# Optimization experiments

Hardware: AMD Instinct MI355X
Metric: run time of the kernel (lower is better)

## Reference

```python
import jax, jax.numpy as jnp
import numpy as np

B, T, D = 2, 1024, 4096
N, K, H = 32, 8, 128  # query heads, kv heads, head_dim
SLOTS = 4096
ROPE_THETA = 500000.0


def apply_rope(x, positions, head_dim, theta):
    # x: [B, heads, T, H], positions: [B, T]
    half = head_dim // 2
    inv_freq = 1.0 / (theta ** (jnp.arange(0, half, dtype=jnp.float32) / half * 2.0 * 0.5 * 2))
    inv_freq = 1.0 / (theta ** (jnp.arange(0, head_dim, 2, dtype=jnp.float32) / head_dim))  # [half]
    ang = positions.astype(jnp.float32)[:, :, None] * inv_freq[None, None, :]  # [B, T, half]
    cos = jnp.cos(ang)[:, None, :, :]  # [B, 1, T, half]
    sin = jnp.sin(ang)[:, None, :, :]
    x1, x2 = x[..., :half], x[..., half:]
    return jnp.concatenate([x1 * cos - x2 * sin, x2 * cos + x1 * sin], axis=-1)


def update_cache(cache, write_indices, kv):
    # cache: [K, SLOTS, H]; kv: [B, K, T, H]; write_indices: [B*T] flat slot ids
    flat = kv.transpose(1, 0, 2, 3).reshape(kv.shape[1], -1, kv.shape[3])  # [K, B*T, H]
    return cache.at[:, write_indices, :].set(flat)


def setup_inputs() -> dict:
    key = jax.random.key(0)
    ks = jax.random.split(key, 6)
    scale = 0.02
    x = jax.random.normal(ks[0], (B, T, D), jnp.float32)
    wq = jax.random.normal(ks[1], (N, D, H), jnp.float32) * scale
    wk = jax.random.normal(ks[2], (K, D, H), jnp.float32) * scale
    wv = jax.random.normal(ks[3], (K, D, H), jnp.float32) * scale
    wo = jax.random.normal(ks[4], (N, H, D), jnp.float32) * scale
    positions = jnp.tile(jnp.arange(T, dtype=jnp.int32)[None, :], (B, 1))
    k_cache = jnp.zeros((K, SLOTS, H), jnp.float32)
    v_cache = jnp.zeros((K, SLOTS, H), jnp.float32)
    write_indices = jnp.arange(B * T, dtype=jnp.int32)
    return {"x": x, "positions": positions, "wq": wq, "wk": wk, "wv": wv,
            "wo": wo, "k_cache": k_cache, "v_cache": v_cache,
            "write_indices": write_indices}


def reference(x, positions, wq, wk, wv, wo, k_cache, v_cache, write_indices):
    # QKV projections
    q = jnp.einsum('btd,ndh->bnth', x, wq)          # [B, N, T, H]
    k = jnp.einsum('btd,kdh->bkth', x, wk)          # [B, K, T, H]
    v = jnp.einsum('btd,kdh->bkth', x, wv)
    # RoPE, then scale q (matches module: rope before scaling)
    q = apply_rope(q, positions, H, ROPE_THETA) * (H ** -0.5)
    k = apply_rope(k, positions, H, ROPE_THETA)
    # KV-cache scatter update (prefill path)
    k_cache_new = update_cache(k_cache, write_indices, k)
    v_cache_new = update_cache(v_cache, write_indices, v)
    # GQA repeat + causal flash attention
    rep = N // K
    kr = jnp.repeat(k, rep, axis=1)                 # [B, N, T, H]
    vr = jnp.repeat(v, rep, axis=1)
    scores = jnp.einsum('bnth,bnsh->bnts', q, kr)   # [B, N, T, T]
    causal = jnp.tril(jnp.ones((T, T), bool))
    scores = jnp.where(causal[None, None], scores, jnp.finfo(scores.dtype).min)
    probs = jax.nn.softmax(scores, axis=-1)
    attn = jnp.einsum('bnts,bnsh->bnth', probs, vr) # [B, N, T, H]
    o = jnp.einsum('bnth,nhd->btd', attn, wo)       # [B, T, D]
    return (k_cache_new, v_cache_new, o)
```

## Files before the change

### kernel.cpp

```cpp
#include <hip/hip_runtime.h>

typedef unsigned short u16;
typedef float fx4 __attribute__((ext_vector_type(4)));
typedef __bf16 bfx8 __attribute__((ext_vector_type(8)));

#define NSLOTS 4096
#define NEG_INF (-1e30f)
#define QSCALE 0.12751879523486166f

__device__ __forceinline__ u16 f2bf(float f) {
    union { float f; unsigned u; } v; v.f = f;
    unsigned u = v.u;
    unsigned r = (u + 0x7FFFu + ((u >> 16) & 1u)) >> 16;
    return (u16)r;
}
__device__ __forceinline__ float bf2f(u16 h) {
    union { unsigned u; float f; } v; v.u = ((unsigned)h) << 16; return v.f;
}
__device__ __forceinline__ void gll16(const void* g, void* l) {
    __builtin_amdgcn_global_load_lds((__attribute__((address_space(1))) void*)(g),
                                     (__attribute__((address_space(3))) void*)(l),
                                     16, 0, 0);
}

__device__ __forceinline__ void transpose_body(u16 (*t)[72],
                                               const float* __restrict__ ih,
                                               u16* __restrict__ oh, int R, int C,
                                               int r0, int c0) {
    int tid = threadIdx.x;
    int rr = tid >> 4, c4 = tid & 15;
#pragma unroll
    for (int i = 0; i < 4; ++i) {
        int r = rr + i * 16;
        float4 v = *(const float4*)(ih + (size_t)(r0 + r) * C + c0 + c4 * 4);
        t[c4 * 4 + 0][r] = f2bf(v.x);
        t[c4 * 4 + 1][r] = f2bf(v.y);
        t[c4 * 4 + 2][r] = f2bf(v.z);
        t[c4 * 4 + 3][r] = f2bf(v.w);
    }
    __syncthreads();
    int rr2 = tid >> 3, c8 = tid & 7;
#pragma unroll
    for (int i = 0; i < 2; ++i) {
        int r = rr2 + i * 32;
        *(uint4*)(oh + (size_t)(c0 + r) * R + r0 + c8 * 8) = *(uint4*)&t[r][c8 * 8];
    }
}

__global__ __launch_bounds__(256) void prep(
    const float* __restrict__ x, const float* __restrict__ wq,
    const float* __restrict__ wk, const float* __restrict__ wv,
    const float* __restrict__ wo, const float* __restrict__ kc,
    const float* __restrict__ vc, u16* __restrict__ x_bf,
    u16* __restrict__ wqkvT, u16* __restrict__ woT, float* __restrict__ cache_out) {
    __shared__ __align__(16) u16 t[64][72];
    int id = blockIdx.x;
    int tid = threadIdx.x;
    if (id < 4096) {
        int f4i = id * 512 + tid * 2;
        const float4* src = (id < 2048) ? (const float4*)kc + f4i
                                        : (const float4*)vc + (f4i - 1048576);
        float4 a = src[0], b = src[1];
        float4* dst = (float4*)cache_out + f4i;
        dst[0] = a;
        dst[1] = b;
    } else if (id < 8192) {
        int i = ((id - 4096) * 256 + tid) * 8;
        float4 a = *(const float4*)(x + i);
        float4 b = *(const float4*)(x + i + 4);
        u16 tmp[8] = {f2bf(a.x), f2bf(a.y), f2bf(a.z), f2bf(a.w),
                      f2bf(b.x), f2bf(b.y), f2bf(b.z), f2bf(b.w)};
        *(uint4*)(x_bf + i) = *(uint4*)tmp;
    } else if (id < 14336) {
        int id3 = id - 8192;
        int z = id3 >> 7;
        int rem = id3 & 127;
        int by = rem >> 1, bx = rem & 1;
        const float* in = (z < 32) ? wq + (size_t)z * 524288
                                   : (z < 40) ? wk + (size_t)(z - 32) * 524288
                                              : wv + (size_t)(z - 40) * 524288;
        transpose_body(t, in, wqkvT + (size_t)z * 524288, 4096, 128, by * 64,
                       bx * 64);
    } else {
        int id4 = id - 14336;
        int bx = id4 & 63, by = id4 >> 6;
        transpose_body(t, wo, woT, 4096, 4096, by * 64, bx * 64);
    }
}

template <int OUTF32>
__global__ __launch_bounds__(256) void gemm_bt(const u16* __restrict__ A,
                                               const u16* __restrict__ Bt,
                                               void* __restrict__ Cv,
                                               int M, int N, int Kd) {
    __shared__ __align__(16) u16 As[128 * 64];
    __shared__ __align__(16) u16 Bs[128 * 64];
    const int tid = threadIdx.x;
    const int lane = tid & 63;
    const int wave = tid >> 6;
    const int wm = (wave >> 1) * 64;
    const int wn = (wave & 1) * 64;
    const int m0 = blockIdx.y * 128;
    const int n0 = blockIdx.x * 128;
    const int quad = lane >> 4;
    const int l15 = lane & 15;
    const int srow = lane >> 3;
    const int sc8 = (lane & 7) ^ srow;

    fx4 zero = {0.f, 0.f, 0.f, 0.f};
    fx4 acc[4][4];
#pragma unroll
    for (int i = 0; i < 4; ++i)
#pragma unroll
        for (int j = 0; j < 4; ++j) acc[i][j] = zero;

    for (int k0 = 0; k0 < Kd; k0 += 64) {
        __syncthreads();
#pragma unroll
        for (int i = 0; i < 4; ++i) {
            int c = wave * 4 + i;
            gll16(A + (size_t)(m0 + c * 8 + srow) * Kd + (k0 + sc8 * 8), &As[c * 512]);
            gll16(Bt + (size_t)(n0 + c * 8 + srow) * Kd + (k0 + sc8 * 8), &Bs[c * 512]);
        }
        __syncthreads();
#pragma unroll
        for (int ks = 0; ks < 2; ++ks) {
            bfx8 af[4], bf[4];
#pragma unroll
            for (int t = 0; t < 4; ++t) {
                int row = wm + t * 16 + l15;
                int r7 = row & 7;
                int k8 = (ks * 4 + quad) ^ r7;
                af[t] = *(const bfx8*)&As[(row >> 3) * 512 + r7 * 64 + k8 * 8];
                int rowb = wn + t * 16 + l15;
                int r7b = rowb & 7;
                int k8b = (ks * 4 + quad) ^ r7b;
                bf[t] = *(const bfx8*)&Bs[(rowb >> 3) * 512 + r7b * 64 + k8b * 8];
            }
#pragma unroll
            for (int tm = 0; tm < 4; ++tm)
#pragma unroll
                for (int tn = 0; tn < 4; ++tn)
                    acc[tm][tn] = __builtin_amdgcn_mfma_f32_16x16x32_bf16(
                        af[tm], bf[tn], acc[tm][tn], 0, 0, 0);
        }
    }
#pragma unroll
    for (int tm = 0; tm < 4; ++tm)
#pragma unroll
        for (int tn = 0; tn < 4; ++tn) {
            int col = n0 + wn + tn * 16 + l15;
#pragma unroll
            for (int r = 0; r < 4; ++r) {
                int row = m0 + wm + tm * 16 + quad * 4 + r;
                if (OUTF32)
                    ((float*)Cv)[(size_t)row * N + col] = acc[tm][tn][r];
                else
                    ((u16*)Cv)[(size_t)row * N + col] = f2bf(acc[tm][tn][r]);
            }
        }
}

__global__ __launch_bounds__(256) void rope_tv(
    const u16* __restrict__ qkv, const int* __restrict__ positions,
    const int* __restrict__ wi, u16* __restrict__ qb, u16* __restrict__ kb,
    float* __restrict__ kcache, float* __restrict__ vcache, u16* __restrict__ vt) {
    __shared__ __align__(16) u16 Ts[64 * 64];
    int id = blockIdx.x;
    int tid = threadIdx.x;
    if (id < 24576) {
        int m = id / 12;
        int j2 = (id % 12) * 256 + tid;
        int head = j2 >> 6;
        int hp = (j2 & 63) * 2;
        int b = m >> 10, t = m & 1023;
        const u16* row = qkv + (size_t)m * 6144 + head * 128;
        unsigned sv = *(const unsigned*)(row + hp);
        float v0 = bf2f((u16)sv), v1 = bf2f((u16)(sv >> 16));
        if (head < 40) {
            int i = hp & 63;
            float p = (float)positions[m];
            float ang0 = p * __expf(-0.20503693f * (float)i);
            float ang1 = ang0 * 0.81461709f;
            float c0, s0, c1, s1;
            __sincosf(ang0, &s0, &c0);
            __sincosf(ang1, &s1, &c1);
            unsigned ov = *(const unsigned*)(row + (hp ^ 64));
            float w0 = bf2f((u16)ov), w1 = bf2f((u16)(ov >> 16));
            float o0, o1;
            if (hp < 64) { o0 = v0 * c0 - w0 * s0; o1 = v1 * c1 - w1 * s1; }
            else         { o0 = v0 * c0 + w0 * s0; o1 = v1 * c1 + w1 * s1; }
            if (head < 32) {
                o0 *= QSCALE; o1 *= QSCALE;
                u16 t2[2] = {f2bf(o0), f2bf(o1)};
                *(unsigned*)(qb + ((size_t)(b * 32 + head) * 1024 + t) * 128 + hp) =
                    *(unsigned*)t2;
            } else {
                int kh = head - 32;
                u16 t2[2] = {f2bf(o0), f2bf(o1)};
                *(unsigned*)(kb + ((size_t)(b * 8 + kh) * 1024 + t) * 128 + hp) =
                    *(unsigned*)t2;
                float2 f2 = {o0, o1};
                *(float2*)(kcache + ((size_t)kh * NSLOTS + wi[m]) * 128 + hp) = f2;
            }
        } else {
            int kh = head - 40;
            float2 f2 = {v0, v1};
            *(float2*)(vcache + ((size_t)kh * NSLOTS + wi[m]) * 128 + hp) = f2;
        }
    } else {
        int idx = id - 24576;
        int tt = idx & 15;
        int hh = (idx >> 4) & 1;
        int bkh = idx >> 5;
        int bq = bkh >> 3, kh = bkh & 7;
        const u16* src =
            qkv + (size_t)(bq * 1024 + tt * 64) * 6144 + 5120 + kh * 128 + hh * 64;
        {
            int r = tid >> 3, c8 = tid & 7;
#pragma unroll
            for (int i = 0; i < 2; ++i) {
                int rr = r + i * 32;
                *(uint4*)&Ts[rr * 64 + ((c8 ^ (rr & 7)) * 8)] =
                    *(const uint4*)(src + (size_t)rr * 6144 + c8 * 8);
            }
        }
        __syncthreads();
        int h = tid & 63, t8 = tid >> 6;
        int h8 = h >> 3, h7 = h & 7;
        u16* dst =
            vt + (size_t)bkh * 131072 + (size_t)(hh * 64 + h) * 1024 + tt * 64;
#pragma unroll
        for (int i = 0; i < 2; ++i) {
            int tb = t8 + i * 4;
            u16 tmp[8];
#pragma unroll
            for (int j = 0; j < 8; ++j)
                tmp[j] = Ts[(tb * 8 + j) * 64 + ((h8 ^ j) * 8 + h7)];
            *(uint4*)(dst + tb * 8) = *(uint4*)tmp;
        }
    }
}

__global__ __launch_bounds__(256) void flash_attn(const u16* __restrict__ qb,
                                                  const u16* __restrict__ kb,
                                                  const u16* __restrict__ vt,
                                                  u16* __restrict__ attn) {
    const int qt = blockIdx.x;
    const int n = blockIdx.y;
    const int b = blockIdx.z;
    const int kh = n >> 2;
    const int tid = threadIdx.x;
    const int lane = tid & 63;
    const int wave = tid >> 6;
    const int quad = lane >> 4;
    const int l15 = lane & 15;

    __shared__ __align__(16) u16 Ks[64 * 128];
    __shared__ __align__(16) u16 Vs[128 * 64];
    __shared__ __align__(16) u16 Ps[4][16 * 72];

    const u16* qbase =
        qb + ((size_t)(b * 32 + n) * 1024 + qt * 64 + wave * 16 + l15) * 128;
    bfx8 qf[4];
#pragma unroll
    for (int ks = 0; ks < 4; ++ks)
        qf[ks] = *(const bfx8*)(qbase + ks * 32 + quad * 8);

    const u16* kbase = kb + (size_t)(b * 8 + kh) * 131072;
    const u16* vbase = vt + (size_t)(b * 8 + kh) * 131072;

    const int kl = wave * 4 + (lane >> 4);
    const int kh8 = (lane & 15) ^ (kl & 7);
    const int hl = wave * 8 + (lane >> 3);
    const int vk8 = (lane & 7) ^ (hl & 7);

    fx4 zero = {0.f, 0.f, 0.f, 0.f};
    fx4 o[8];
#pragma unroll
    for (int i = 0; i < 8; ++i) o[i] = zero;
    float mrow[4], lrow[4];
#pragma unroll
    for (int r = 0; r < 4; ++r) { mrow[r] = NEG_INF; lrow[r] = 0.f; }

    for (int kt = 0; kt <= qt; ++kt) {
        __syncthreads();
        const u16* ksrc = kbase + (size_t)kt * 64 * 128;
        const u16* vsrc = vbase + kt * 64;
#pragma unroll
        for (int i = 0; i < 4; ++i)
            gll16(ksrc + (size_t)(i * 16 + kl) * 128 + kh8 * 8,
                  &Ks[(i * 16 + wave * 4) * 128]);
#pragma unroll
        for (int i = 0; i < 4; ++i)
            gll16(vsrc + (size_t)(i * 32 + hl) * 1024 + vk8 * 8,
                  &Vs[(i * 32 + wave * 8) * 64]);
        __syncthreads();

        fx4 sAcc[4];
#pragma unroll
        for (int t = 0; t < 4; ++t) sAcc[t] = zero;
#pragma unroll
        for (int ks = 0; ks < 4; ++ks)
#pragma unroll
            for (int tn = 0; tn < 4; ++tn) {
                int key = tn * 16 + l15;
                bfx8 kf =
                    *(const bfx8*)&Ks[key * 128 + (((ks * 4 + quad) ^ (key & 7)) * 8)];
                sAcc[tn] = __builtin_amdgcn_mfma_f32_16x16x32_bf16(qf[ks], kf,
                                                                   sAcc[tn], 0, 0, 0);
            }
        if (kt == qt) {
#pragma unroll
            for (int tn = 0; tn < 4; ++tn)
#pragma unroll
                for (int r = 0; r < 4; ++r) {
                    int qrow = wave * 16 + quad * 4 + r;
                    int krow = tn * 16 + l15;
                    if (krow > qrow) sAcc[tn][r] = NEG_INF;
                }
        }
        float alpha[4];
#pragma unroll
        for (int r = 0; r < 4; ++r) {
            float mx = fmaxf(fmaxf(sAcc[0][r], sAcc[1][r]),
                             fmaxf(sAcc[2][r], sAcc[3][r]));
#pragma unroll
            for (int d = 1; d < 16; d <<= 1) mx = fmaxf(mx, __shfl_xor(mx, d));
            float mnew = fmaxf(mrow[r], mx);
            alpha[r] = exp2f(mrow[r] - mnew);
            mrow[r] = mnew;
            float rs = 0.f;
#pragma unroll
            for (int tn = 0; tn < 4; ++tn) {
                float p = exp2f(sAcc[tn][r] - mnew);
                sAcc[tn][r] = p;
                rs += p;
            }
#pragma unroll
            for (int d = 1; d < 16; d <<= 1) rs += __shfl_xor(rs, d);
            lrow[r] = lrow[r] * alpha[r] + rs;
        }
#pragma unroll
        for (int tn = 0; tn < 4; ++tn)
#pragma unroll
            for (int r = 0; r < 4; ++r)
                Ps[wave][(quad * 4 + r) * 72 + tn * 16 + l15] = f2bf(sAcc[tn][r]);
#pragma unroll
        for (int ht = 0; ht < 8; ++ht)
#pragma unroll
            for (int r = 0; r < 4; ++r) o[ht][r] *= alpha[r];
#pragma unroll
        for (int ks2 = 0; ks2 < 2; ++ks2) {
            bfx8 pf = *(const bfx8*)&Ps[wave][l15 * 72 + ks2 * 32 + quad * 8];
#pragma unroll
            for (int ht = 0; ht < 8; ++ht) {
                int h = ht * 16 + l15;
                bfx8 vf =
                    *(const bfx8*)&Vs[h * 64 + (((ks2 * 4 + quad) ^ (h & 7)) * 8)];
                o[ht] = __builtin_amdgcn_mfma_f32_16x16x32_bf16(pf, vf, o[ht], 0, 0, 0);
            }
        }
    }
    float inv_l[4];
#pragma unroll
    for (int r = 0; r < 4; ++r) inv_l[r] = 1.f / lrow[r];
#pragma unroll
    for (int ht = 0; ht < 8; ++ht)
#pragma unroll
        for (int r = 0; r < 4; ++r) {
            int t = qt * 64 + wave * 16 + quad * 4 + r;
            int col = n * 128 + ht * 16 + l15;
            attn[((size_t)(b * 1024 + t)) * 4096 + col] = f2bf(o[ht][r] * inv_l[r]);
        }
}

extern "C" void kernel_launch(void* const* d_in, const int* in_sizes, int n_in,
                              void* d_out, int out_size, void* d_ws, size_t ws_size,
                              hipStream_t stream) {
    const float* x = (const float*)d_in[0];
    const int* pos = (const int*)d_in[1];
    const float* wq = (const float*)d_in[2];
    const float* wk = (const float*)d_in[3];
    const float* wv = (const float*)d_in[4];
    const float* wo = (const float*)d_in[5];
    const float* kc = (const float*)d_in[6];
    const float* vc = (const float*)d_in[7];
    const int* wi = (const int*)d_in[8];

    float* kc_out = (float*)d_out;
    float* vc_out = kc_out + 4194304;
    float* o_out = vc_out + 4194304;

    u16* wsp = (u16*)d_ws;
    u16* x_bf  = wsp;
    u16* wqkvT = x_bf + 8388608;
    u16* woT   = wqkvT + 25165824;
    u16* qkv   = woT + 16777216;
    u16* qbuf  = qkv + 12582912;
    u16* kbuf  = qbuf + 8388608;
    u16* vtb   = kbuf + 2097152;
    u16* attn  = vtb + 2097152;

    prep<<<18432, 256, 0, stream>>>(x, wq, wk, wv, wo, kc, vc, x_bf, wqkvT, woT,
                                    kc_out);
    gemm_bt<0><<<dim3(48, 16), 256, 0, stream>>>(x_bf, wqkvT, qkv, 2048, 6144, 4096);
    rope_tv<<<25088, 256, 0, stream>>>(qkv, pos, wi, qbuf, kbuf, kc_out, vc_out, vtb);
    flash_attn<<<dim3(16, 32, 2), 256, 0, stream>>>(qbuf, kbuf, vtb, attn);
    gemm_bt<1><<<dim3(32, 16), 256, 0, stream>>>(attn, woT, o_out, 2048, 4096, 4096);
}
```

Before: 543.7 us.

## Pair causal query tiles per block, swizzle transpose LDS, defer row-sum reduction

Flash attention now launches half as many blocks. Each block handles query tile p and then tile 15-p, so every block does the same amount of causal work instead of some blocks doing far more than others. The per-iteration row-sum shuffle reduction is deferred to a single reduction at the end. The weight transpose in prep uses an XOR-swizzled LDS layout to avoid bank conflicts, and the cache copy switches to coalesced strided float4 accesses. The grid shrinks to 512 blocks, which may reduce occupancy on a GPU with many CUs.

```diff
diff --git a/kernel.cpp b/kernel.cpp
--- a/kernel.cpp
+++ b/kernel.cpp
@@ -23,7 +23,7 @@
                                      16, 0, 0);
 }
 
-__device__ __forceinline__ void transpose_body(u16 (*t)[72],
+__device__ __forceinline__ void transpose_body(u16* __restrict__ t,
                                                const float* __restrict__ ih,
                                                u16* __restrict__ oh, int R, int C,
                                                int r0, int c0) {
@@ -31,19 +31,22 @@
     int rr = tid >> 4, c4 = tid & 15;
 #pragma unroll
     for (int i = 0; i < 4; ++i) {
-        int r = rr + i * 16;
-        float4 v = *(const float4*)(ih + (size_t)(r0 + r) * C + c0 + c4 * 4);
-        t[c4 * 4 + 0][r] = f2bf(v.x);
-        t[c4 * 4 + 1][r] = f2bf(v.y);
-        t[c4 * 4 + 2][r] = f2bf(v.z);
-        t[c4 * 4 + 3][r] = f2bf(v.w);
+        int b = rr + i * 16;
+        float4 v = *(const float4*)(ih + (size_t)(r0 + b) * C + c0 + c4 * 4);
+        u16 vals[4] = {f2bf(v.x), f2bf(v.y), f2bf(v.z), f2bf(v.w)};
+#pragma unroll
+        for (int j = 0; j < 4; ++j) {
+            int a = c4 * 4 + j;
+            t[a * 72 + (((b >> 3) ^ (a & 7)) << 3) + (b & 7)] = vals[j];
+        }
     }
     __syncthreads();
     int rr2 = tid >> 3, c8 = tid & 7;
 #pragma unroll
     for (int i = 0; i < 2; ++i) {
-        int r = rr2 + i * 32;
-        *(uint4*)(oh + (size_t)(c0 + r) * R + r0 + c8 * 8) = *(uint4*)&t[r][c8 * 8];
+        int a = rr2 + i * 32;
+        *(uint4*)(oh + (size_t)(c0 + a) * R + r0 + c8 * 8) =
+            *(uint4*)&t[a * 72 + ((c8 ^ (a & 7)) << 3)];
     }
 }
 
@@ -53,17 +56,17 @@
     const float* __restrict__ wo, const float* __restrict__ kc,
     const float* __restrict__ vc, u16* __restrict__ x_bf,
     u16* __restrict__ wqkvT, u16* __restrict__ woT, float* __restrict__ cache_out) {
-    __shared__ __align__(16) u16 t[64][72];
+    __shared__ __align__(16) u16 t[64 * 72];
     int id = blockIdx.x;
     int tid = threadIdx.x;
     if (id < 4096) {
-        int f4i = id * 512 + tid * 2;
+        int f4i = id * 512 + tid;
         const float4* src = (id < 2048) ? (const float4*)kc + f4i
                                         : (const float4*)vc + (f4i - 1048576);
-        float4 a = src[0], b = src[1];
+        float4 a = src[0], b = src[256];
         float4* dst = (float4*)cache_out + f4i;
         dst[0] = a;
-        dst[1] = b;
+        dst[256] = b;
     } else if (id < 8192) {
         int i = ((id - 4096) * 256 + tid) * 8;
         float4 a = *(const float4*)(x + i);
@@ -89,10 +92,10 @@
 }
 
 template <int OUTF32>
-__global__ __launch_bounds__(256) void gemm_bt(const u16* __restrict__ A,
-                                               const u16* __restrict__ Bt,
-                                               void* __restrict__ Cv,
-                                               int M, int N, int Kd) {
+__device__ __forceinline__ void gemm_core(const u16* __restrict__ A,
+                                          const u16* __restrict__ Bt,
+                                          void* __restrict__ Cv,
+                                          int M, int N, int Kd) {
     __shared__ __align__(16) u16 As[128 * 64];
     __shared__ __align__(16) u16 Bs[128 * 64];
     const int tid = threadIdx.x;
@@ -159,6 +162,19 @@
                     ((u16*)Cv)[(size_t)row * N + col] = f2bf(acc[tm][tn][r]);
             }
         }
+}
+
+__global__ __launch_bounds__(256) void gemm_qkv(const u16* __restrict__ A,
+                                                const u16* __restrict__ Bt,
+                                                u16* __restrict__ C, int M, int N,
+                                                int Kd) {
+    gemm_core<0>(A, Bt, C, M, N, Kd);
+}
+__global__ __launch_bounds__(256) void gemm_out(const u16* __restrict__ A,
+                                                const u16* __restrict__ Bt,
+                                                float* __restrict__ C, int M, int N,
+                                                int Kd) {
+    gemm_core<1>(A, Bt, C, M, N, Kd);
 }
 
 __global__ __launch_bounds__(256) void rope_tv(
@@ -246,7 +262,7 @@
                                                   const u16* __restrict__ kb,
                                                   const u16* __restrict__ vt,
                                                   u16* __restrict__ attn) {
-    const int qt = blockIdx.x;
+    const int p = blockIdx.x;
     const int n = blockIdx.y;
     const int b = blockIdx.z;
     const int kh = n >> 2;
@@ -260,13 +276,6 @@
     __shared__ __align__(16) u16 Vs[128 * 64];
     __shared__ __align__(16) u16 Ps[4][16 * 72];
 
-    const u16* qbase =
-        qb + ((size_t)(b * 32 + n) * 1024 + qt * 64 + wave * 16 + l15) * 128;
-    bfx8 qf[4];
-#pragma unroll
-    for (int ks = 0; ks < 4; ++ks)
-        qf[ks] = *(const bfx8*)(qbase + ks * 32 + quad * 8);
-
     const u16* kbase = kb + (size_t)(b * 8 + kh) * 131072;
     const u16* vbase = vt + (size_t)(b * 8 + kh) * 131072;
 
@@ -276,103 +285,118 @@
     const int vk8 = (lane & 7) ^ (hl & 7);
 
     fx4 zero = {0.f, 0.f, 0.f, 0.f};
-    fx4 o[8];
-#pragma unroll
-    for (int i = 0; i < 8; ++i) o[i] = zero;
-    float mrow[4], lrow[4];
-#pragma unroll
-    for (int r = 0; r < 4; ++r) { mrow[r] = NEG_INF; lrow[r] = 0.f; }
-
-    for (int kt = 0; kt <= qt; ++kt) {
-        __syncthreads();
-        const u16* ksrc = kbase + (size_t)kt * 64 * 128;
-        const u16* vsrc = vbase + kt * 64;
-#pragma unroll
-        for (int i = 0; i < 4; ++i)
-            gll16(ksrc + (size_t)(i * 16 + kl) * 128 + kh8 * 8,
-                  &Ks[(i * 16 + wave * 4) * 128]);
-#pragma unroll
-        for (int i = 0; i < 4; ++i)
-            gll16(vsrc + (size_t)(i * 32 + hl) * 1024 + vk8 * 8,
-                  &Vs[(i * 32 + wave * 8) * 64]);
-        __syncthreads();
-
-        fx4 sAcc[4];
-#pragma unroll
-        for (int t = 0; t < 4; ++t) sAcc[t] = zero;
+
+    for (int ph = 0; ph < 2; ++ph) {
+        const int qt = ph ? (15 - p) : p;
+        const u16* qbase =
+            qb + ((size_t)(b * 32 + n) * 1024 + qt * 64 + wave * 16 + l15) * 128;
+        bfx8 qf[4];
 #pragma unroll
         for (int ks = 0; ks < 4; ++ks)
-#pragma unroll
-            for (int tn = 0; tn < 4; ++tn) {
-                int key = tn * 16 + l15;
-                bfx8 kf =
-                    *(const bfx8*)&Ks[key * 128 + (((ks * 4 + quad) ^ (key & 7)) * 8)];
-                sAcc[tn] = __builtin_amdgcn_mfma_f32_16x16x32_bf16(qf[ks], kf,
-                                                                   sAcc[tn], 0, 0, 0);
-            }
-        if (kt == qt) {
+            qf[ks] = *(const bfx8*)(qbase + ks * 32 + quad * 8);
+
+        fx4 o[8];
+#pragma unroll
+        for (int i = 0; i < 8; ++i) o[i] = zero;
+        float mrow[4], lrow[4];
+#pragma unroll
+        for (int r = 0; r < 4; ++r) { mrow[r] = NEG_INF; lrow[r] = 0.f; }
+
+        for (int kt = 0; kt <= qt; ++kt) {
+            __syncthreads();
+            const u16* ksrc = kbase + (size_t)kt * 64 * 128;
+            const u16* vsrc = vbase + kt * 64;
+#pragma unroll
+            for (int i = 0; i < 4; ++i)
+                gll16(ksrc + (size_t)(i * 16 + kl) * 128 + kh8 * 8,
+                      &Ks[(i * 16 + wave * 4) * 128]);
+#pragma unroll
+            for (int i = 0; i < 4; ++i)
+                gll16(vsrc + (size_t)(i * 32 + hl) * 1024 + vk8 * 8,
+                      &Vs[(i * 32 + wave * 8) * 64]);
+            __syncthreads();
+
+            fx4 sAcc[4];
+#pragma unroll
+            for (int t = 0; t < 4; ++t) sAcc[t] = zero;
+#pragma unroll
+            for (int ks = 0; ks < 4; ++ks)
+#pragma unroll
+                for (int tn = 0; tn < 4; ++tn) {
+                    int key = tn * 16 + l15;
+                    bfx8 kf = *(const bfx8*)&Ks[key * 128 +
+                                                (((ks * 4 + quad) ^ (key & 7)) * 8)];
+                    sAcc[tn] = __builtin_amdgcn_mfma_f32_16x16x32_bf16(
+                        qf[ks], kf, sAcc[tn], 0, 0, 0);
+                }
+            if (kt == qt) {
+#pragma unroll
+                for (int tn = 0; tn < 4; ++tn)
+#pragma unroll
+                    for (int r = 0; r < 4; ++r) {
+                        int qrow = wave * 16 + quad * 4 + r;
+                        int krow = tn * 16 + l15;
+                        if (krow > qrow) sAcc[tn][r] = NEG_INF;
+                    }
+            }
+            float alpha[4];
+#pragma unroll
+            for (int r = 0; r < 4; ++r) {
+                float mx = fmaxf(fmaxf(sAcc[0][r], sAcc[1][r]),
+                                 fmaxf(sAcc[2][r], sAcc[3][r]));
+#pragma unroll
+                for (int d = 1; d < 16; d <<= 1) mx = fmaxf(mx, __shfl_xor(mx, d));
+                float mnew = fmaxf(mrow[r], mx);
+                alpha[r] = exp2f(mrow[r] - mnew);
+                mrow[r] = mnew;
+                float rs = 0.f;
+#pragma unroll
+                for (int tn = 0; tn < 4; ++tn) {
+                    float pv = exp2f(sAcc[tn][r] - mnew);
+                    sAcc[tn][r] = pv;
+                    rs += pv;
+                }
+                lrow[r] = lrow[r] * alpha[r] + rs;
+            }
 #pragma unroll
             for (int tn = 0; tn < 4; ++tn)
 #pragma unroll
-                for (int r = 0; r < 4; ++r) {
-                    int qrow = wave * 16 + quad * 4 + r;
-                    int krow = tn * 16 + l15;
-                    if (krow > qrow) sAcc[tn][r] = NEG_INF;
+                for (int r = 0; r < 4; ++r)
+                    Ps[wave][(quad * 4 + r) * 72 + tn * 16 + l15] = f2bf(sAcc[tn][r]);
+#pragma unroll
+            for (int ht = 0; ht < 8; ++ht)
+#pragma unroll
+                for (int r = 0; r < 4; ++r) o[ht][r] *= alpha[r];
+#pragma unroll
+            for (int ks2 = 0; ks2 < 2; ++ks2) {
+                bfx8 pf = *(const bfx8*)&Ps[wave][l15 * 72 + ks2 * 32 + quad * 8];
+#pragma unroll
+                for (int ht = 0; ht < 8; ++ht) {
+                    int h = ht * 16 + l15;
+                    bfx8 vf =
+                        *(const bfx8*)&Vs[h * 64 + (((ks2 * 4 + quad) ^ (h & 7)) * 8)];
+                    o[ht] = __builtin_amdgcn_mfma_f32_16x16x32_bf16(pf, vf, o[ht],
+                                                                    0, 0, 0);
                 }
-        }
-        float alpha[4];
+            }
+        }
+        float inv_l[4];
 #pragma unroll
         for (int r = 0; r < 4; ++r) {
-            float mx = fmaxf(fmaxf(sAcc[0][r], sAcc[1][r]),
-                             fmaxf(sAcc[2][r], sAcc[3][r]));
-#pragma unroll
-            for (int d = 1; d < 16; d <<= 1) mx = fmaxf(mx, __shfl_xor(mx, d));
-            float mnew = fmaxf(mrow[r], mx);
-            alpha[r] = exp2f(mrow[r] - mnew);
-            mrow[r] = mnew;
-            float rs = 0.f;
-#pragma unroll
-            for (int tn = 0; tn < 4; ++tn) {
-                float p = exp2f(sAcc[tn][r] - mnew);
-                sAcc[tn][r] = p;
-                rs += p;
-            }
-#pragma unroll
-            for (int d = 1; d < 16; d <<= 1) rs += __shfl_xor(rs, d);
-            lrow[r] = lrow[r] * alpha[r] + rs;
-        }
-#pragma unroll
-        for (int tn = 0; tn < 4; ++tn)
-#pragma unroll
-            for (int r = 0; r < 4; ++r)
-                Ps[wave][(quad * 4 + r) * 72 + tn * 16 + l15] = f2bf(sAcc[tn][r]);
+            float s = lrow[r];
+#pragma unroll
+            for (int d = 1; d < 16; d <<= 1) s += __shfl_xor(s, d);
+            inv_l[r] = 1.f / s;
+        }
 #pragma unroll
         for (int ht = 0; ht < 8; ++ht)
 #pragma unroll
-            for (int r = 0; r < 4; ++r) o[ht][r] *= alpha[r];
-#pragma unroll
-        for (int ks2 = 0; ks2 < 2; ++ks2) {
-            bfx8 pf = *(const bfx8*)&Ps[wave][l15 * 72 + ks2 * 32 + quad * 8];
-#pragma unroll
-            for (int ht = 0; ht < 8; ++ht) {
-                int h = ht * 16 + l15;
-                bfx8 vf =
-                    *(const bfx8*)&Vs[h * 64 + (((ks2 * 4 + quad) ^ (h & 7)) * 8)];
-                o[ht] = __builtin_amdgcn_mfma_f32_16x16x32_bf16(pf, vf, o[ht], 0, 0, 0);
-            }
-        }
-    }
-    float inv_l[4];
-#pragma unroll
-    for (int r = 0; r < 4; ++r) inv_l[r] = 1.f / lrow[r];
-#pragma unroll
-    for (int ht = 0; ht < 8; ++ht)
-#pragma unroll
-        for (int r = 0; r < 4; ++r) {
-            int t = qt * 64 + wave * 16 + quad * 4 + r;
-            int col = n * 128 + ht * 16 + l15;
-            attn[((size_t)(b * 1024 + t)) * 4096 + col] = f2bf(o[ht][r] * inv_l[r]);
-        }
+            for (int r = 0; r < 4; ++r) {
+                int t = qt * 64 + wave * 16 + quad * 4 + r;
+                int col = n * 128 + ht * 16 + l15;
+                attn[((size_t)(b * 1024 + t)) * 4096 + col] = f2bf(o[ht][r] * inv_l[r]);
+            }
+    }
 }
 
 extern "C" void kernel_launch(void* const* d_in, const int* in_sizes, int n_in,
@@ -404,8 +428,8 @@
 
     prep<<<18432, 256, 0, stream>>>(x, wq, wk, wv, wo, kc, vc, x_bf, wqkvT, woT,
                                     kc_out);
-    gemm_bt<0><<<dim3(48, 16), 256, 0, stream>>>(x_bf, wqkvT, qkv, 2048, 6144, 4096);
+    gemm_qkv<<<dim3(48, 16), 256, 0, stream>>>(x_bf, wqkvT, qkv, 2048, 6144, 4096);
     rope_tv<<<25088, 256, 0, stream>>>(qkv, pos, wi, qbuf, kbuf, kc_out, vc_out, vtb);
-    flash_attn<<<dim3(16, 32, 2), 256, 0, stream>>>(qbuf, kbuf, vtb, attn);
-    gemm_bt<1><<<dim3(32, 16), 256, 0, stream>>>(attn, woT, o_out, 2048, 4096, 4096);
-}
+    flash_attn<<<dim3(8, 32, 2), 256, 0, stream>>>(qbuf, kbuf, vtb, attn);
+    gemm_out<<<dim3(32, 16), 256, 0, stream>>>(attn, woT, o_out, 2048, 4096, 4096);
+}
```

New measurement: 516.0 us. 1.05x faster.
